# Kernel tuning notes

Measured on AMD Instinct MI355X. Metric: run time of the kernel, lower is better.

## Reference

```python
import jax, jax.numpy as jnp
import numpy as np

# Model dims: H features, N half-state-size, R low-rank, CH output channels, KL kernel length
H, N, R, CH, KL = 512, 64, 1, 1, 4096


def setup_inputs() -> dict:
    key = jax.random.key(0)
    ks = jax.random.split(key, 8)
    log_dt = jax.random.uniform(ks[0], (H,), minval=float(np.log(1e-3)), maxval=float(np.log(1e-1)), dtype=jnp.float32)
    # Hurwitz-like poles: negative real part, HiPPO-like imaginary ladder
    w_re = -0.5 - jax.random.uniform(ks[1], (H, N), dtype=jnp.float32)
    w_im = jnp.broadcast_to(np.float32(np.pi) * jnp.arange(N, dtype=jnp.float32), (H, N))
    B_re = jax.random.normal(ks[2], (1, H, N), dtype=jnp.float32)
    B_im = jax.random.normal(ks[3], (1, H, N), dtype=jnp.float32)
    # small low-rank correction keeps the Woodbury denominator away from zero
    P_re = 0.1 * jax.random.normal(ks[4], (R, H, N), dtype=jnp.float32)
    P_im = 0.1 * jax.random.normal(ks[5], (R, H, N), dtype=jnp.float32)
    C_re = jax.random.normal(ks[6], (CH, H, N), dtype=jnp.float32)
    C_im = jax.random.normal(ks[7], (CH, H, N), dtype=jnp.float32)
    return dict(log_dt=log_dt, w_re=w_re, w_im=w_im, B_re=B_re, B_im=B_im,
                P_re=P_re, P_im=P_im, C_re=C_re, C_im=C_im, L=KL)


def _kernel(log_dt, w_re, w_im, B_re, B_im, P_re, P_im, C_re, C_im, L):
    dt = jnp.exp(log_dt)                                   # (H,)
    w = (w_re + 1j * w_im) * dt[:, None]                   # (H,N) discretized poles w*dt
    B = B_re + 1j * B_im                                   # (1,H,N)
    P = P_re + 1j * P_im                                   # (R,H,N)
    Q = jnp.conj(P)                                        # hurwitz=False path: Q = conj(P)
    C = C_re + 1j * C_im                                   # (CH,H,N)

    Lf = L // 2 + 1
    kk = jnp.arange(Lf)
    omega = jnp.exp((-2j * np.pi) * kk / L)                # FFT roots of unity (complex64)
    den = 1.0 + omega
    # Nyquist node (omega = -1) handled analytically below; guard the division
    safe_den = jnp.where(jnp.abs(den) < 1e-6, jnp.ones_like(den), den)
    z = 2.0 * (1.0 - omega) / safe_den                     # bilinear-transform nodes

    Bc = jnp.concatenate([B, P], axis=0)                   # (1+R,H,N)
    Cc = jnp.concatenate([C, Q], axis=0)                   # (CH+R,H,N)
    v = Bc[:, None] * Cc[None]                             # (1+R,CH+R,H,N)

    # Cauchy kernel: r[a,b,h,l] = sum_n v[a,b,h,n] / (z[l] - w[h,n])
    recip = 1.0 / (z[None, None, :] - w[:, :, None])       # (H,N,Lf)
    r = jnp.einsum('abhn,hnl->abhl', v, recip)             # (1+R,CH+R,H,Lf)
    r = r * dt[None, None, :, None]

    # rank-1 Woodbury correction
    k_f = r[:-1, :-1] - r[:-1, -1:] * r[-1:, :-1] / (1.0 + r[-1:, -1:])
    k_f = k_f * 2.0 / safe_den

    if L % 2 == 0:
        # analytic z -> inf limit at the Nyquist node: dt/2 * sum_n v00
        nyq = 0.5 * dt[None, None, :] * jnp.sum(v[:-1, :-1], axis=-1)  # (1,CH,H)
        k_f = k_f.at[..., -1].set(nyq)

    k = jnp.fft.irfft(k_f, n=L, axis=-1)[..., :L]          # (1,CH,H,L) real
    return k[-1]                                           # (CH,H,L)


def reference(log_dt, w_re, w_im, B_re, B_im, P_re, P_im, C_re, C_im, L):
    return _kernel(log_dt, w_re, w_im, B_re, B_im, P_re, P_im, C_re, C_im, L)
```

## Files before the change

### kernel.cpp

```cpp
#include <hip/hip_runtime.h>
#include <hip/hip_bf16.h>
#include <math.h>


#define HH   512
#define NN   64
#define LLEN 4096
#define MM   2048
#define NTHREADS 512
#define ZPAD(i) ((i) + ((i) >> 4))

typedef float v2f __attribute__((ext_vector_type(2)));

__device__ __forceinline__ float sinr(float r) { return __builtin_amdgcn_sinf(r); }
__device__ __forceinline__ float cosr(float r) { return __builtin_amdgcn_cosf(r); }
__device__ __forceinline__ float rcpf(float x) { return __builtin_amdgcn_rcpf(x); }

__device__ __forceinline__ void cauchy_step(
    const v2f tv, const v2f mwi, const v2f nr, const v2f wr2,
    const v2f v00r, const v2f v00i, const v2f v01r, const v2f v01i,
    const v2f v10r, const v2f v10i, const v2f v11,
    v2f& a00r, v2f& a00i, v2f& a01r, v2f& a01i,
    v2f& a10r, v2f& a10i, v2f& a11r, v2f& a11i)
{
    const v2f dim = __builtin_elementwise_fma(tv, (v2f){2.0f, 2.0f}, mwi);
    const v2f den = __builtin_elementwise_fma(dim, dim, wr2);
    const float ip = rcpf(den.x * den.y);
    v2f inv; inv.x = den.y * ip; inv.y = den.x * ip;
    const v2f ur = nr * inv;
    const v2f ui = -(dim * inv);
    a00r = __builtin_elementwise_fma( v00r, ur, a00r);
    a00r = __builtin_elementwise_fma(-v00i, ui, a00r);
    a00i = __builtin_elementwise_fma( v00r, ui, a00i);
    a00i = __builtin_elementwise_fma( v00i, ur, a00i);
    a01r = __builtin_elementwise_fma( v01r, ur, a01r);
    a01r = __builtin_elementwise_fma(-v01i, ui, a01r);
    a01i = __builtin_elementwise_fma( v01r, ui, a01i);
    a01i = __builtin_elementwise_fma( v01i, ur, a01i);
    a10r = __builtin_elementwise_fma( v10r, ur, a10r);
    a10r = __builtin_elementwise_fma(-v10i, ui, a10r);
    a10i = __builtin_elementwise_fma( v10r, ui, a10i);
    a10i = __builtin_elementwise_fma( v10i, ur, a10i);
    a11r = __builtin_elementwise_fma( v11,  ur, a11r);
    a11i = __builtin_elementwise_fma( v11,  ui, a11i);
}

__device__ __forceinline__ void woodbury_K(
    const v2f tv,
    const v2f a00r, const v2f a00i, const v2f a01r, const v2f a01i,
    const v2f a10r, const v2f a10i, const v2f a11r, const v2f a11i,
    v2f& Kr, v2f& Ki)
{
    const v2f dr = a11r + 1.0f;
    const v2f di = a11i;
    const v2f dd = __builtin_elementwise_fma(dr, dr, di * di);
    v2f dinv; dinv.x = rcpf(dd.x); dinv.y = rcpf(dd.y);
    const v2f numr = a01r * a10r - a01i * a10i;
    const v2f numi = a01r * a10i + a01i * a10r;
    const v2f cr = (numr * dr + numi * di) * dinv;
    const v2f ci = (numi * dr - numr * di) * dinv;
    const v2f Wr = a00r - cr;
    const v2f Wi = a00i - ci;
    Kr = __builtin_elementwise_fma(-tv, Wi, Wr);
    Ki = __builtin_elementwise_fma( tv, Wr, Wi);
}

__global__ __launch_bounds__(NTHREADS, 4) void ssknplr_kernel(
    const float* __restrict__ log_dt,
    const float* __restrict__ w_re, const float* __restrict__ w_im,
    const float* __restrict__ B_re, const float* __restrict__ B_im,
    const float* __restrict__ P_re, const float* __restrict__ P_im,
    const float* __restrict__ C_re, const float* __restrict__ C_im,
    float* __restrict__ out)
{
    __shared__ float4 s_p4[NN][5];
    __shared__ float2 s_Z[ZPAD(MM) + 1];

    const int h   = blockIdx.x;
    const int tid = threadIdx.x;

    if (tid < NN) {
        const int n   = tid;
        const int idx = h * NN + n;
        const float dt = expf(log_dt[h]);
        const float wr = w_re[idx] * dt;
        const float wi = w_im[idx] * dt;
        const float Br = B_re[idx], Bi = B_im[idx];
        const float Pr = P_re[idx], Pi = P_im[idx];
        const float Cr = C_re[idx], Ci = C_im[idx];
        const float v00r = dt * (Br * Cr - Bi * Ci);
        const float v00i = dt * (Br * Ci + Bi * Cr);
        const float v01r = dt * (Br * Pr + Bi * Pi);
        const float v01i = dt * (Bi * Pr - Br * Pi);
        const float v10r = dt * (Pr * Cr - Pi * Ci);
        const float v10i = dt * (Pr * Ci + Pi * Cr);
        const float v11  = dt * (Pr * Pr + Pi * Pi);
        s_p4[n][0] = make_float4(-wi, -wi, -wr, -wr);
        s_p4[n][1] = make_float4(wr * wr, wr * wr, v00r, v00r);
        s_p4[n][2] = make_float4(v00i, v00i, v01r, v01r);
        s_p4[n][3] = make_float4(v01i, v01i, v10r, v10r);
        s_p4[n][4] = make_float4(v10i, v10i, v11, v11);
    }
    __syncthreads();

    v2f tvA, tvB;
    {
        const float rA0 = (float)tid           * (1.0f / 8192.0f);
        const float rA1 = (float)(tid + 1024)  * (1.0f / 8192.0f);
        const float rB0 = (float)(tid + 512)   * (1.0f / 8192.0f);
        const float rB1 = (float)(tid + 1536)  * (1.0f / 8192.0f);
        tvA.x = sinr(rA0) * rcpf(cosr(rA0));
        tvA.y = sinr(rA1) * rcpf(cosr(rA1));
        tvB.x = sinr(rB0) * rcpf(cosr(rB0));
        tvB.y = sinr(rB1) * rcpf(cosr(rB1));
    }

    v2f A00r = {0.f,0.f}, A00i = {0.f,0.f}, A01r = {0.f,0.f}, A01i = {0.f,0.f};
    v2f A10r = {0.f,0.f}, A10i = {0.f,0.f}, A11r = {0.f,0.f}, A11i = {0.f,0.f};
    v2f B00r = {0.f,0.f}, B00i = {0.f,0.f}, B01r = {0.f,0.f}, B01i = {0.f,0.f};
    v2f B10r = {0.f,0.f}, B10i = {0.f,0.f}, B11r = {0.f,0.f}, B11i = {0.f,0.f};

    for (int n = 0; n < NN; ++n) {
        const float4 f0 = s_p4[n][0];
        const float4 f1 = s_p4[n][1];
        const float4 f2 = s_p4[n][2];
        const float4 f3 = s_p4[n][3];
        const float4 f4 = s_p4[n][4];
        const v2f mwi  = {f0.x, f0.y}, nr   = {f0.z, f0.w};
        const v2f wr2  = {f1.x, f1.y}, v00r = {f1.z, f1.w};
        const v2f v00i = {f2.x, f2.y}, v01r = {f2.z, f2.w};
        const v2f v01i = {f3.x, f3.y}, v10r = {f3.z, f3.w};
        const v2f v10i = {f4.x, f4.y}, v11  = {f4.z, f4.w};
        cauchy_step(tvA, mwi, nr, wr2, v00r, v00i, v01r, v01i, v10r, v10i, v11,
                    A00r, A00i, A01r, A01i, A10r, A10i, A11r, A11i);
        cauchy_step(tvB, mwi, nr, wr2, v00r, v00i, v01r, v01i, v10r, v10i, v11,
                    B00r, B00i, B01r, B01i, B10r, B10i, B11r, B11i);
    }

    {
        v2f Kr, Ki;
        woodbury_K(tvA, A00r, A00i, A01r, A01i, A10r, A10i, A11r, A11i, Kr, Ki);
        s_Z[ZPAD(tid)]        = make_float2(Kr.x, (tid == 0) ? 0.0f : Ki.x);
        s_Z[ZPAD(tid + 1024)] = make_float2(Kr.y, Ki.y);
    }
    {
        v2f Kr, Ki;
        woodbury_K(tvB, B00r, B00i, B01r, B01i, B10r, B10i, B11r, B11i, Kr, Ki);
        s_Z[ZPAD(tid + 512)]  = make_float2(Kr.x, Ki.x);
        s_Z[ZPAD(tid + 1536)] = make_float2(Kr.y, Ki.y);
    }
    if (tid == 0) {
        float sr = 0.f;
        for (int n = 0; n < NN; ++n) sr += s_p4[n][1].z;
        s_Z[ZPAD(MM)] = make_float2(0.5f * sr, 0.0f);
    }
    __syncthreads();

    #pragma unroll
    for (int q = 0; q < 2; ++q) {
        const int k = tid + (q << 9);
        if (k == 0) {
            const float a = s_Z[ZPAD(0)].x;
            const float b = s_Z[ZPAD(MM)].x;
            s_Z[ZPAD(0)] = make_float2(0.5f * (a + b), 0.5f * (a - b));
            const float2 km = s_Z[ZPAD(MM / 2)];
            s_Z[ZPAD(MM / 2)] = make_float2(km.x, -km.y);
        } else {
            const float2 Ka = s_Z[ZPAD(k)];
            const float2 Kb = s_Z[ZPAD(MM - k)];
            const float rk = (float)k * (1.0f / 4096.0f);
            const float sk = sinr(rk);
            const float ck = cosr(rk);
            const float Pr = 0.5f * (Ka.x + Kb.x), Pi = 0.5f * (Ka.y - Kb.y);
            const float Dr = 0.5f * (Ka.x - Kb.x), Di = 0.5f * (Ka.y + Kb.y);
            const float al = sk * Dr + ck * Di;
            const float be = ck * Dr - sk * Di;
            s_Z[ZPAD(k)]      = make_float2(Pr - al, Pi + be);
            s_Z[ZPAD(MM - k)] = make_float2(Pr + al, be - Pi);
        }
    }
    __syncthreads();

    for (int s = 10; s >= 1; s -= 2) {
        const int H = 1 << s;
        const int Q = H >> 1;
        const float scale = rcpf((float)(2 * H));
        {
            const int b    = tid;
            const int j    = b & (Q - 1);
            const int base = ((b >> (s - 1)) << (s + 1)) + j;
            const int i0 = base, i1 = base + Q, i2 = base + H, i3 = base + H + Q;
            const float rev = (float)j * scale;
            const float c  = cosr(rev);
            const float sn = sinr(rev);
            const float wbr = c * c - sn * sn;
            const float wbi = 2.0f * c * sn;
            const float2 u0 = s_Z[ZPAD(i0)];
            const float2 u1 = s_Z[ZPAD(i1)];
            const float2 u2 = s_Z[ZPAD(i2)];
            const float2 u3 = s_Z[ZPAD(i3)];
            const float a0r = u0.x + u2.x, a0i = u0.y + u2.y;
            const float d0r = u0.x - u2.x, d0i = u0.y - u2.y;
            const float a1r = u1.x + u3.x, a1i = u1.y + u3.y;
            const float d1r = u1.x - u3.x, d1i = u1.y - u3.y;
            const float e0r = d0r * c  - d0i * sn, e0i = d0r * sn + d0i * c;
            const float e1r = -(d1r * sn) - d1i * c, e1i = d1r * c - d1i * sn;
            s_Z[ZPAD(i0)] = make_float2(a0r + a1r, a0i + a1i);
            const float t0r = a0r - a1r, t0i = a0i - a1i;
            s_Z[ZPAD(i1)] = make_float2(t0r * wbr - t0i * wbi, t0r * wbi + t0i * wbr);
            s_Z[ZPAD(i2)] = make_float2(e0r + e1r, e0i + e1i);
            const float t1r = e0r - e1r, t1i = e0i - e1i;
            s_Z[ZPAD(i3)] = make_float2(t1r * wbr - t1i * wbi, t1r * wbi + t1i * wbr);
        }
        __syncthreads();
    }
    {
        #pragma unroll
        for (int q = 0; q < 2; ++q) {
            const int b  = tid + (q << 9);
            const int i0 = b << 1, i1 = i0 | 1;
            const float2 u = s_Z[ZPAD(i0)];
            const float2 v = s_Z[ZPAD(i1)];
            s_Z[ZPAD(i0)] = make_float2(u.x + v.x, u.y + v.y);
            s_Z[ZPAD(i1)] = make_float2(u.x - v.x, u.y - v.y);
        }
    }
    __syncthreads();

    const float scale = 1.0f / (float)MM;
    float2* o2 = (float2*)out + (size_t)h * MM;
    #pragma unroll
    for (int q = 0; q < 4; ++q) {
        const int m = tid + (q << 9);
        const int r = (int)(__brev((unsigned)m) >> 21);
        const float2 z = s_Z[ZPAD(r)];
        o2[m] = make_float2(z.x * scale, z.y * scale);
    }
}

extern "C" void kernel_launch(void* const* d_in, const int* in_sizes, int n_in,
                              void* d_out, int out_size, void* d_ws, size_t ws_size,
                              hipStream_t stream) {
    const float* log_dt = (const float*)d_in[0];
    const float* w_re   = (const float*)d_in[1];
    const float* w_im   = (const float*)d_in[2];
    const float* B_re   = (const float*)d_in[3];
    const float* B_im   = (const float*)d_in[4];
    const float* P_re   = (const float*)d_in[5];
    const float* P_im   = (const float*)d_in[6];
    const float* C_re   = (const float*)d_in[7];
    const float* C_im   = (const float*)d_in[8];
    float* out = (float*)d_out;

    ssknplr_kernel<<<dim3(HH), dim3(NTHREADS), 0, stream>>>(
        log_dt, w_re, w_im, B_re, B_im, P_re, P_im, C_re, C_im, out);
}
```

Measured before the change: 36.62 us.

## Pair each thread's frequency nodes k and M-k to fuse real-FFT post-processing in registers

Each thread now evaluates the Cauchy sum at mirrored nodes k and M-k instead of k and k+1024. The tangent of the mirrored node is taken as the reciprocal cotangent from the same sin/cos pair, so fewer trig calls are needed. The real-to-complex untangling butterfly can then run straight on register values, which removes one shared-memory round trip and one block barrier. The Nyquist and DC special cases are folded into thread 0.

```diff
diff --git a/kernel.cpp b/kernel.cpp
--- a/kernel.cpp
+++ b/kernel.cpp
@@ -105,14 +105,14 @@
 
     v2f tvA, tvB;
     {
-        const float rA0 = (float)tid           * (1.0f / 8192.0f);
-        const float rA1 = (float)(tid + 1024)  * (1.0f / 8192.0f);
-        const float rB0 = (float)(tid + 512)   * (1.0f / 8192.0f);
-        const float rB1 = (float)(tid + 1536)  * (1.0f / 8192.0f);
-        tvA.x = sinr(rA0) * rcpf(cosr(rA0));
-        tvA.y = sinr(rA1) * rcpf(cosr(rA1));
-        tvB.x = sinr(rB0) * rcpf(cosr(rB0));
-        tvB.y = sinr(rB1) * rcpf(cosr(rB1));
+        const float rA = (float)tid         * (1.0f / 8192.0f);
+        const float rB = (float)(tid + 512) * (1.0f / 8192.0f);
+        const float sA = sinr(rA), cA = cosr(rA);
+        const float sB = sinr(rB), cB = cosr(rB);
+        tvA.x = sA * rcpf(cA);
+        tvA.y = (tid == 0) ? 1.0f : cA * rcpf(sA);
+        tvB.x = sB * rcpf(cB);
+        tvB.y = cB * rcpf(sB);
     }
 
     v2f A00r = {0.f,0.f}, A00i = {0.f,0.f}, A01r = {0.f,0.f}, A01i = {0.f,0.f};
@@ -140,44 +140,36 @@
     {
         v2f Kr, Ki;
         woodbury_K(tvA, A00r, A00i, A01r, A01i, A10r, A10i, A11r, A11i, Kr, Ki);
-        s_Z[ZPAD(tid)]        = make_float2(Kr.x, (tid == 0) ? 0.0f : Ki.x);
-        s_Z[ZPAD(tid + 1024)] = make_float2(Kr.y, Ki.y);
+        if (tid == 0) {
+            float sr = 0.f;
+            for (int n = 0; n < NN; ++n) sr += s_p4[n][1].z;
+            const float KN = 0.5f * sr;
+            s_Z[ZPAD(0)]    = make_float2(0.5f * (Kr.x + KN), 0.5f * (Kr.x - KN));
+            s_Z[ZPAD(1024)] = make_float2(Kr.y, -Ki.y);
+        } else {
+            const int k = tid, Mk = MM - tid;
+            const float rk = (float)k * (1.0f / 4096.0f);
+            const float sk = sinr(rk), ck = cosr(rk);
+            const float Pr = 0.5f * (Kr.x + Kr.y), Pi = 0.5f * (Ki.x - Ki.y);
+            const float Dr = 0.5f * (Kr.x - Kr.y), Di = 0.5f * (Ki.x + Ki.y);
+            const float al = sk * Dr + ck * Di;
+            const float be = ck * Dr - sk * Di;
+            s_Z[ZPAD(k)]  = make_float2(Pr - al, Pi + be);
+            s_Z[ZPAD(Mk)] = make_float2(Pr + al, be - Pi);
+        }
     }
     {
         v2f Kr, Ki;
         woodbury_K(tvB, B00r, B00i, B01r, B01i, B10r, B10i, B11r, B11i, Kr, Ki);
-        s_Z[ZPAD(tid + 512)]  = make_float2(Kr.x, Ki.x);
-        s_Z[ZPAD(tid + 1536)] = make_float2(Kr.y, Ki.y);
-    }
-    if (tid == 0) {
-        float sr = 0.f;
-        for (int n = 0; n < NN; ++n) sr += s_p4[n][1].z;
-        s_Z[ZPAD(MM)] = make_float2(0.5f * sr, 0.0f);
-    }
-    __syncthreads();
-
-    #pragma unroll
-    for (int q = 0; q < 2; ++q) {
-        const int k = tid + (q << 9);
-        if (k == 0) {
-            const float a = s_Z[ZPAD(0)].x;
-            const float b = s_Z[ZPAD(MM)].x;
-            s_Z[ZPAD(0)] = make_float2(0.5f * (a + b), 0.5f * (a - b));
-            const float2 km = s_Z[ZPAD(MM / 2)];
-            s_Z[ZPAD(MM / 2)] = make_float2(km.x, -km.y);
-        } else {
-            const float2 Ka = s_Z[ZPAD(k)];
-            const float2 Kb = s_Z[ZPAD(MM - k)];
-            const float rk = (float)k * (1.0f / 4096.0f);
-            const float sk = sinr(rk);
-            const float ck = cosr(rk);
-            const float Pr = 0.5f * (Ka.x + Kb.x), Pi = 0.5f * (Ka.y - Kb.y);
-            const float Dr = 0.5f * (Ka.x - Kb.x), Di = 0.5f * (Ka.y + Kb.y);
-            const float al = sk * Dr + ck * Di;
-            const float be = ck * Dr - sk * Di;
-            s_Z[ZPAD(k)]      = make_float2(Pr - al, Pi + be);
-            s_Z[ZPAD(MM - k)] = make_float2(Pr + al, be - Pi);
-        }
+        const int k = 512 + tid, Mk = 1536 - tid;
+        const float rk = (float)k * (1.0f / 4096.0f);
+        const float sk = sinr(rk), ck = cosr(rk);
+        const float Pr = 0.5f * (Kr.x + Kr.y), Pi = 0.5f * (Ki.x - Ki.y);
+        const float Dr = 0.5f * (Kr.x - Kr.y), Di = 0.5f * (Ki.x + Ki.y);
+        const float al = sk * Dr + ck * Di;
+        const float be = ck * Dr - sk * Di;
+        s_Z[ZPAD(k)]  = make_float2(Pr - al, Pi + be);
+        s_Z[ZPAD(Mk)] = make_float2(Pr + al, be - Pi);
     }
     __syncthreads();
 
```

Result: no change. 36.40 us (-0.6%).
